# Kernel tuning notes

Hardware: AMD Instinct MI355X
Metric: run time of the kernel (lower is better)

Reference implementation:

```python
import jax, jax.numpy as jnp
import numpy as np

DIM = 2048
H = 16        # num query heads
HK = 2        # num kv heads
D = DIM // H  # head_dim = 128
G = H // HK   # q heads per kv head = 8
SCALE = 1.0 / np.sqrt(D)


def setup_inputs() -> dict:
    key = jax.random.key(0)
    ks = jax.random.split(key, 9)
    xavier = lambda k, fi, fo: jax.random.uniform(k, (fi, fo), jnp.float32,
                                                  -np.sqrt(6.0 / (fi + fo)), np.sqrt(6.0 / (fi + fo)))
    return {
        "x": jax.random.normal(ks[0], (2, 2048, DIM), jnp.float32),
        "Wq": xavier(ks[1], DIM, H * D),  "bq": jnp.zeros((H * D,), jnp.float32),
        "Wk": xavier(ks[2], DIM, HK * D), "bk": jnp.zeros((HK * D,), jnp.float32),
        "Wv": xavier(ks[3], DIM, HK * D), "bv": jnp.zeros((HK * D,), jnp.float32),
        "Wo": xavier(ks[4], H * D, DIM),  "bo": jnp.zeros((DIM,), jnp.float32),
    }


def reference(x, Wq, bq, Wk, bk, Wv, bv, Wo, bo):
    B, T, C = x.shape
    # projections; q grouped as (kv_head, group) so repeat_interleave becomes a broadcast
    q = (x @ Wq + bq).reshape(B, T, HK, G, D)   # [B,T,Hk,G,D]
    k = (x @ Wk + bk).reshape(B, T, HK, D)      # [B,T,Hk,D]
    v = (x @ Wv + bv).reshape(B, T, HK, D)
    # scores: [B,Hk,G,Tq,Tk] — shared K broadcast across the G query heads per kv head
    scores = jnp.einsum('bqhgd,bshd->bhgqs', q, k) * SCALE
    scores = jnp.clip(scores, -100.0, 100.0)
    attn = jax.nn.softmax(scores, axis=-1)
    out = jnp.einsum('bhgqs,bshd->bqhgd', attn, v).reshape(B, T, H * D)
    return out @ Wo + bo
```

## Files before the change

kernel.cpp:

```cpp
#include <hip/hip_runtime.h>
#include <cstdint>

typedef __bf16 bf16x8 __attribute__((ext_vector_type(8)));
typedef float floatx4 __attribute__((ext_vector_type(4)));
typedef unsigned short u16;
typedef unsigned int u32;

#define SCALE2 0.1275434297677098f
#define CLIP2  144.26950408889634f

__device__ __forceinline__ u16 f2bf(float f) {
  union { float f; u32 i; } v; v.f = f;
  u32 r = v.i + 0x7fffu + ((v.i >> 16) & 1u);
  return (u16)(r >> 16);
}

__device__ __forceinline__ void gll16(const void* g, void* l) {
  __builtin_amdgcn_global_load_lds(
      (const __attribute__((address_space(1))) u32*)g,
      (__attribute__((address_space(3))) u32*)l, 16, 0, 0);
}

__global__ __launch_bounds__(256) void convert_bf16(
    const float* __restrict__ src, u16* __restrict__ dst, int n4) {
  int i = blockIdx.x * 256 + threadIdx.x;
  if (i >= n4) return;
  float4 v = ((const float4*)src)[i];
  ushort4 o;
  o.x = f2bf(v.x); o.y = f2bf(v.y); o.z = f2bf(v.z); o.w = f2bf(v.w);
  ((ushort4*)dst)[i] = o;
}

__global__ __launch_bounds__(256) void transpose_cat(
    const float* __restrict__ W0, const float* __restrict__ W1,
    const float* __restrict__ W2,
    int n1, int n2, int ld0, int ld1, int ld2, int K, u16* __restrict__ Bt) {
  __shared__ u16 tile[32][33];
  const int k0 = blockIdx.x * 32, n0 = blockIdx.y * 32;
  const float* src; int ld, nb;
  if (n0 < n1)      { src = W0; ld = ld0; nb = n0; }
  else if (n0 < n2) { src = W1; ld = ld1; nb = n0 - n1; }
  else              { src = W2; ld = ld2; nb = n0 - n2; }
  const int tx = threadIdx.x, ty = threadIdx.y;
#pragma unroll
  for (int i = 0; i < 4; i++) {
    int k = ty + i * 8;
    tile[k][tx] = f2bf(src[(size_t)(k0 + k) * ld + nb + tx]);
  }
  __syncthreads();
#pragma unroll
  for (int i = 0; i < 4; i++) {
    int n = ty + i * 8;
    Bt[(size_t)(n0 + n) * K + k0 + tx] = tile[tx][n];
  }
}

template <int EPI>
__global__ __launch_bounds__(256) void gemm_bt(
    const u16* __restrict__ A, const u16* __restrict__ Bt,
    const float* __restrict__ bias0, const float* __restrict__ bias1,
    const float* __restrict__ bias2,
    u16* __restrict__ out0, u16* __restrict__ out1, u16* __restrict__ out2,
    float* __restrict__ outf,
    int M, int N, int K) {
  __shared__ u16 As[2][128][32];
  __shared__ u16 Bs[2][128][32];
  const int tid  = threadIdx.x;
  const int w    = tid >> 6, L = tid & 63, ln = L & 15, quad = L >> 4;
  const int m0   = blockIdx.y * 128, n0 = blockIdx.x * 128;
  const int mw   = (w & 1) * 64, nw = (w >> 1) * 64;
  const int sr = w * 32 + (L >> 2), sc = (L & 3) * 8;
  const u16* ga = &A [(size_t)(m0 + sr) * K + sc];
  const u16* gb = &Bt[(size_t)(n0 + sr) * K + sc];
  floatx4 acc[4][4] = {};
  const int nk = K >> 5;

  gll16(ga, &As[0][w * 32][0]);
  gll16(ga + (size_t)16 * K, &As[0][w * 32 + 16][0]);
  gll16(gb, &Bs[0][w * 32][0]);
  gll16(gb + (size_t)16 * K, &Bs[0][w * 32 + 16][0]);

  for (int i = 0; i < nk; i++) {
    const int cur = i & 1;
    __syncthreads();
    if (i + 1 < nk) {
      const int kt = (i + 1) << 5;
      gll16(ga + kt, &As[cur ^ 1][w * 32][0]);
      gll16(ga + (size_t)16 * K + kt, &As[cur ^ 1][w * 32 + 16][0]);
      gll16(gb + kt, &Bs[cur ^ 1][w * 32][0]);
      gll16(gb + (size_t)16 * K + kt, &Bs[cur ^ 1][w * 32 + 16][0]);
    }
    bf16x8 af[4], bf[4];
#pragma unroll
    for (int mb = 0; mb < 4; mb++) af[mb] = *(const bf16x8*)&As[cur][mw + mb * 16 + ln][quad * 8];
#pragma unroll
    for (int nb = 0; nb < 4; nb++) bf[nb] = *(const bf16x8*)&Bs[cur][nw + nb * 16 + ln][quad * 8];
#pragma unroll
    for (int mb = 0; mb < 4; mb++)
#pragma unroll
      for (int nb = 0; nb < 4; nb++)
        acc[mb][nb] = __builtin_amdgcn_mfma_f32_16x16x32_bf16(af[mb], bf[nb], acc[mb][nb], 0, 0, 0);
  }

#pragma unroll
  for (int mb = 0; mb < 4; mb++) {
#pragma unroll
    for (int nb = 0; nb < 4; nb++) {
#pragma unroll
      for (int r = 0; r < 4; r++) {
        const int m = m0 + mw + mb * 16 + quad * 4 + r;
        const int n = n0 + nw + nb * 16 + ln;
        float v = acc[mb][nb][r];
        if constexpr (EPI == 0) {
          if (n < 2048) {
            v = (v + bias0[n]) * SCALE2;
            out0[(size_t)m * 2048 + n] = f2bf(v);
          } else if (n < 2304) {
            const int j = n - 2048;
            v += bias1[j];
            out1[(size_t)m * 256 + j] = f2bf(v);
          } else {
            const int j = n - 2304;
            v += bias2[j];
            const int b = m >> 11, t = m & 2047;
            out2[((size_t)(b * 256 + j)) * 2048 + t] = f2bf(v);
          }
        } else {
          v += bias0[n];
          outf[(size_t)m * (size_t)N + n] = v;
        }
      }
    }
  }
}

__global__ __launch_bounds__(512, 4) void attn_kernel(
    const u16* __restrict__ Q, const u16* __restrict__ K,
    const u16* __restrict__ Vt, u16* __restrict__ O) {
  __shared__ u16 Ksh[2][16 * 512];
  __shared__ u16 Vsh[2][16 * 512];
  const int tid = threadIdx.x;
  const int w = tid >> 6, L = tid & 63, ln = L & 15, quad = L >> 4;
  const int qt = blockIdx.x, h = blockIdx.y, b = blockIdx.z;
  const int hk = h >> 3;
  const size_t qrow0 = (size_t)b * 2048 + qt * 128 + w * 16;

  const u16* Kbase = K + (size_t)b * 2048 * 256 + hk * 128;
  const u16* Vbase = Vt + (size_t)(b * 2 + hk) * 128 * 2048;

  const int fk0 = w * 2;
  const int kkc0 = fk0 >> 2, knb0 = fk0 & 3;
  const int kkc1 = (fk0 + 1) >> 2, knb1 = (fk0 + 1) & 3;
  const int vkc0 = fk0 >> 3, vnb0 = fk0 & 7;
  const int vkc1 = (fk0 + 1) >> 3, vnb1 = (fk0 + 1) & 7;
  const u16* gK0 = Kbase + (size_t)(knb0 * 16 + ln) * 256 + kkc0 * 32 + quad * 8;
  const u16* gK1 = Kbase + (size_t)(knb1 * 16 + ln) * 256 + kkc1 * 32 + quad * 8;
  const u16* gV0 = Vbase + (size_t)(vnb0 * 16 + ln) * 2048 + vkc0 * 32 + quad * 8;
  const u16* gV1 = Vbase + (size_t)(vnb1 * 16 + ln) * 2048 + vkc1 * 32 + quad * 8;

  bf16x8 qf[4];
#pragma unroll
  for (int kc = 0; kc < 4; kc++)
    qf[kc] = *(const bf16x8*)&Q[(qrow0 + ln) * 2048 + h * 128 + kc * 32 + quad * 8];

  floatx4 oT[8] = {};
  float mrow = -1e30f, lrow = 0.f;

  gll16(gK0, &Ksh[0][(size_t)fk0 * 512]);
  gll16(gK1, &Ksh[0][(size_t)(fk0 + 1) * 512]);
  gll16(gV0, &Vsh[0][(size_t)fk0 * 512]);
  gll16(gV1, &Vsh[0][(size_t)(fk0 + 1) * 512]);

  const int s0l = ((L & 16) << 1) + ln;
  const int s1l = s0l + 16;
  const bool hi = (L & 32) != 0;

  for (int i = 0; i < 32; i++) {
    const int cur = i & 1;
    __syncthreads();
    if (i < 31) {
      const int s0 = (i + 1) * 64;
      gll16(gK0 + (size_t)s0 * 256, &Ksh[cur ^ 1][(size_t)fk0 * 512]);
      gll16(gK1 + (size_t)s0 * 256, &Ksh[cur ^ 1][(size_t)(fk0 + 1) * 512]);
      gll16(gV0 + s0, &Vsh[cur ^ 1][(size_t)fk0 * 512]);
      gll16(gV1 + s0, &Vsh[cur ^ 1][(size_t)(fk0 + 1) * 512]);
    }

    floatx4 sf[4] = {};
#pragma unroll
    for (int kc = 0; kc < 4; kc++) {
#pragma unroll
      for (int nb = 0; nb < 4; nb++) {
        bf16x8 kf = *(const bf16x8*)&Ksh[cur][(size_t)(kc * 4 + nb) * 512 + L * 8];
        sf[nb] = __builtin_amdgcn_mfma_f32_16x16x32_bf16(kf, qf[kc], sf[nb], 0, 0, 0);
      }
    }
#pragma unroll
    for (int nb = 0; nb < 4; nb++)
#pragma unroll
      for (int r = 0; r < 4; r++)
        sf[nb][r] = __builtin_amdgcn_fmed3f(sf[nb][r], -CLIP2, CLIP2);

    float mx = sf[0][0];
#pragma unroll
    for (int nb = 0; nb < 4; nb++)
#pragma unroll
      for (int r = 0; r < 4; r++) mx = fmaxf(mx, sf[nb][r]);
    mx = fmaxf(mx, __shfl_xor(mx, 16));
    mx = fmaxf(mx, __shfl_xor(mx, 32));
    const float mn = fmaxf(mrow, mx);
    const float alpha = __builtin_amdgcn_exp2f(mrow - mn);
    mrow = mn;

    float s = 0.f;
    uint2 pk[4];
#pragma unroll
    for (int nb = 0; nb < 4; nb++) {
      float p0 = __builtin_amdgcn_exp2f(sf[nb][0] - mn);
      float p1 = __builtin_amdgcn_exp2f(sf[nb][1] - mn);
      float p2 = __builtin_amdgcn_exp2f(sf[nb][2] - mn);
      float p3 = __builtin_amdgcn_exp2f(sf[nb][3] - mn);
      s += (p0 + p1) + (p2 + p3);
      pk[nb].x = (u32)f2bf(p0) | ((u32)f2bf(p1) << 16);
      pk[nb].y = (u32)f2bf(p2) | ((u32)f2bf(p3) << 16);
    }
    s += __shfl_xor(s, 16);
    s += __shfl_xor(s, 32);
    lrow = lrow * alpha + s;

    if (__ballot(alpha < 1.f)) {
#pragma unroll
      for (int nb = 0; nb < 8; nb++)
#pragma unroll
        for (int r = 0; r < 4; r++) oT[nb][r] *= alpha;
    }

#pragma unroll
    for (int kc = 0; kc < 2; kc++) {
      u32 a0 = pk[2 * kc].x, a1 = pk[2 * kc].y;
      u32 b0 = pk[2 * kc + 1].x, b1 = pk[2 * kc + 1].y;
      u32 t00 = __shfl(a0, s0l), t01 = __shfl(a1, s0l);
      u32 t02 = __shfl(a0, s1l), t03 = __shfl(a1, s1l);
      u32 t10 = __shfl(b0, s0l), t11 = __shfl(b1, s0l);
      u32 t12 = __shfl(b0, s1l), t13 = __shfl(b1, s1l);
      union { u32 u[4]; bf16x8 v; } pb;
      pb.u[0] = hi ? t10 : t00;
      pb.u[1] = hi ? t11 : t01;
      pb.u[2] = hi ? t12 : t02;
      pb.u[3] = hi ? t13 : t03;
#pragma unroll
      for (int nb = 0; nb < 8; nb++) {
        bf16x8 vf = *(const bf16x8*)&Vsh[cur][(size_t)(kc * 8 + nb) * 512 + L * 8];
        oT[nb] = __builtin_amdgcn_mfma_f32_16x16x32_bf16(vf, pb.v, oT[nb], 0, 0, 0);
      }
    }
  }

  const float inv = 1.f / lrow;
  u16* orow = O + (qrow0 + ln) * 2048 + h * 128;
#pragma unroll
  for (int nb = 0; nb < 8; nb++)
#pragma unroll
    for (int r = 0; r < 4; r++)
      orow[nb * 16 + quad * 4 + r] = f2bf(oT[nb][r] * inv);
}

extern "C" void kernel_launch(void* const* d_in, const int* in_sizes, int n_in,
                              void* d_out, int out_size, void* d_ws, size_t ws_size,
                              hipStream_t stream) {
  const float* x  = (const float*)d_in[0];
  const float* Wq = (const float*)d_in[1];
  const float* bq = (const float*)d_in[2];
  const float* Wk = (const float*)d_in[3];
  const float* bk = (const float*)d_in[4];
  const float* Wv = (const float*)d_in[5];
  const float* bv = (const float*)d_in[6];
  const float* Wo = (const float*)d_in[7];
  const float* bo = (const float*)d_in[8];
  float* out = (float*)d_out;

  char* ws = (char*)d_ws;
  u16* xb     = (u16*)(ws);
  u16* Ob     = (u16*)(ws);
  u16* Wqkv_t = (u16*)(ws + 16777216);
  u16* Wot    = (u16*)(ws + 27262976);
  u16* Qb     = (u16*)(ws + 35651584);
  u16* Kb     = (u16*)(ws + 52428800);
  u16* Vtb    = (u16*)(ws + 54525952);
  (void)in_sizes; (void)n_in; (void)out_size; (void)ws_size;

  convert_bf16<<<8192, 256, 0, stream>>>(x, xb, 2097152);

  transpose_cat<<<dim3(64, 80), dim3(32, 8), 0, stream>>>(
      Wq, Wk, Wv, 2048, 2304, 2048, 256, 256, 2048, Wqkv_t);
  transpose_cat<<<dim3(64, 64), dim3(32, 8), 0, stream>>>(
      Wo, Wo, Wo, 2048, 2048, 2048, 2048, 2048, 2048, Wot);

  gemm_bt<0><<<dim3(20, 32), 256, 0, stream>>>(
      xb, Wqkv_t, bq, bk, bv, Qb, Kb, Vtb, nullptr, 4096, 2560, 2048);

  attn_kernel<<<dim3(16, 16, 2), 512, 0, stream>>>(Qb, Kb, Vtb, Ob);

  gemm_bt<1><<<dim3(16, 32), 256, 0, stream>>>(
      Ob, Wot, bo, nullptr, nullptr, nullptr, nullptr, nullptr, out, 4096, 2048, 2048);
}
```

Before: 344.6 us.

## Switch attention to 32x32x16 MFMA with 4 waves and lazy softmax rescale

New measurement: 337.3 us. -2.1%, faster.

```diff
diff --git a/kernel.cpp b/kernel.cpp
--- a/kernel.cpp
+++ b/kernel.cpp
@@ -3,16 +3,24 @@
 
 typedef __bf16 bf16x8 __attribute__((ext_vector_type(8)));
 typedef float floatx4 __attribute__((ext_vector_type(4)));
+typedef float floatx16 __attribute__((ext_vector_type(16)));
 typedef unsigned short u16;
 typedef unsigned int u32;
 
 #define SCALE2 0.1275434297677098f
 #define CLIP2  144.26950408889634f
+#define DEFER  8.0f
 
 __device__ __forceinline__ u16 f2bf(float f) {
   union { float f; u32 i; } v; v.f = f;
   u32 r = v.i + 0x7fffu + ((v.i >> 16) & 1u);
   return (u16)(r >> 16);
+}
+
+__device__ __forceinline__ u32 cvtpk(float lo, float hi) {
+  u32 r;
+  asm("v_cvt_pk_bf16_f32 %0, %1, %2" : "=v"(r) : "v"(lo), "v"(hi));
+  return r;
 }
 
 __device__ __forceinline__ void gll16(const void* g, void* l) {
@@ -134,124 +142,120 @@
   }
 }
 
-__global__ __launch_bounds__(512, 4) void attn_kernel(
+__global__ __launch_bounds__(256, 2) void attn_kernel(
     const u16* __restrict__ Q, const u16* __restrict__ K,
     const u16* __restrict__ Vt, u16* __restrict__ O) {
   __shared__ u16 Ksh[2][16 * 512];
   __shared__ u16 Vsh[2][16 * 512];
   const int tid = threadIdx.x;
-  const int w = tid >> 6, L = tid & 63, ln = L & 15, quad = L >> 4;
+  const int w = tid >> 6, L = tid & 63;
+  const int ln = L & 31, hf = L >> 5;
   const int qt = blockIdx.x, h = blockIdx.y, b = blockIdx.z;
   const int hk = h >> 3;
-  const size_t qrow0 = (size_t)b * 2048 + qt * 128 + w * 16;
+  const size_t qrow0 = (size_t)b * 2048 + qt * 128 + w * 32;
 
   const u16* Kbase = K + (size_t)b * 2048 * 256 + hk * 128;
   const u16* Vbase = Vt + (size_t)(b * 2 + hk) * 128 * 2048;
 
-  const int fk0 = w * 2;
-  const int kkc0 = fk0 >> 2, knb0 = fk0 & 3;
-  const int kkc1 = (fk0 + 1) >> 2, knb1 = (fk0 + 1) & 3;
-  const int vkc0 = fk0 >> 3, vnb0 = fk0 & 7;
-  const int vkc1 = (fk0 + 1) >> 3, vnb1 = (fk0 + 1) & 7;
-  const u16* gK0 = Kbase + (size_t)(knb0 * 16 + ln) * 256 + kkc0 * 32 + quad * 8;
-  const u16* gK1 = Kbase + (size_t)(knb1 * 16 + ln) * 256 + kkc1 * 32 + quad * 8;
-  const u16* gV0 = Vbase + (size_t)(vnb0 * 16 + ln) * 2048 + vkc0 * 32 + quad * 8;
-  const u16* gV1 = Vbase + (size_t)(vnb1 * 16 + ln) * 2048 + vkc1 * 32 + quad * 8;
-
-  bf16x8 qf[4];
-#pragma unroll
-  for (int kc = 0; kc < 4; kc++)
-    qf[kc] = *(const bf16x8*)&Q[(qrow0 + ln) * 2048 + h * 128 + kc * 32 + quad * 8];
-
-  floatx4 oT[8] = {};
+  const u16* gK[4];
+  const u16* gV[4];
+#pragma unroll
+  for (int j = 0; j < 4; j++) {
+    const int fK = 4 * w + j, mb = fK >> 3, kc = fK & 7;
+    gK[j] = Kbase + (size_t)(mb * 32 + ln) * 256 + kc * 16 + hf * 8;
+    const int fV = 4 * w + j, db = fV >> 2, ks = fV & 3;
+    gV[j] = Vbase + (size_t)(db * 32 + ln) * 2048 + ks * 16 + hf * 8;
+  }
+
+  bf16x8 qf[8];
+#pragma unroll
+  for (int kc = 0; kc < 8; kc++)
+    qf[kc] = *(const bf16x8*)&Q[(qrow0 + ln) * 2048 + h * 128 + kc * 16 + hf * 8];
+
+  floatx16 oT[4] = {};
   float mrow = -1e30f, lrow = 0.f;
 
-  gll16(gK0, &Ksh[0][(size_t)fk0 * 512]);
-  gll16(gK1, &Ksh[0][(size_t)(fk0 + 1) * 512]);
-  gll16(gV0, &Vsh[0][(size_t)fk0 * 512]);
-  gll16(gV1, &Vsh[0][(size_t)(fk0 + 1) * 512]);
-
-  const int s0l = ((L & 16) << 1) + ln;
-  const int s1l = s0l + 16;
-  const bool hi = (L & 32) != 0;
+#pragma unroll
+  for (int j = 0; j < 4; j++) {
+    gll16(gK[j], &Ksh[0][(4 * w + j) * 512]);
+    gll16(gV[j], &Vsh[0][(4 * w + j) * 512]);
+  }
 
   for (int i = 0; i < 32; i++) {
     const int cur = i & 1;
     __syncthreads();
     if (i < 31) {
-      const int s0 = (i + 1) * 64;
-      gll16(gK0 + (size_t)s0 * 256, &Ksh[cur ^ 1][(size_t)fk0 * 512]);
-      gll16(gK1 + (size_t)s0 * 256, &Ksh[cur ^ 1][(size_t)(fk0 + 1) * 512]);
-      gll16(gV0 + s0, &Vsh[cur ^ 1][(size_t)fk0 * 512]);
-      gll16(gV1 + s0, &Vsh[cur ^ 1][(size_t)(fk0 + 1) * 512]);
-    }
-
-    floatx4 sf[4] = {};
-#pragma unroll
-    for (int kc = 0; kc < 4; kc++) {
-#pragma unroll
-      for (int nb = 0; nb < 4; nb++) {
-        bf16x8 kf = *(const bf16x8*)&Ksh[cur][(size_t)(kc * 4 + nb) * 512 + L * 8];
-        sf[nb] = __builtin_amdgcn_mfma_f32_16x16x32_bf16(kf, qf[kc], sf[nb], 0, 0, 0);
-      }
-    }
-#pragma unroll
-    for (int nb = 0; nb < 4; nb++)
-#pragma unroll
-      for (int r = 0; r < 4; r++)
-        sf[nb][r] = __builtin_amdgcn_fmed3f(sf[nb][r], -CLIP2, CLIP2);
-
-    float mx = sf[0][0];
-#pragma unroll
-    for (int nb = 0; nb < 4; nb++)
-#pragma unroll
-      for (int r = 0; r < 4; r++) mx = fmaxf(mx, sf[nb][r]);
-    mx = fmaxf(mx, __shfl_xor(mx, 16));
+#pragma unroll
+      for (int j = 0; j < 4; j++) {
+        gll16(gK[j] + (size_t)(i + 1) * 64 * 256, &Ksh[cur ^ 1][(4 * w + j) * 512]);
+        gll16(gV[j] + (size_t)(i + 1) * 64, &Vsh[cur ^ 1][(4 * w + j) * 512]);
+      }
+    }
+
+    floatx16 sf[2] = {};
+#pragma unroll
+    for (int kc = 0; kc < 8; kc++) {
+#pragma unroll
+      for (int mb = 0; mb < 2; mb++) {
+        bf16x8 kf = *(const bf16x8*)&Ksh[cur][(mb * 8 + kc) * 512 + L * 8];
+        sf[mb] = __builtin_amdgcn_mfma_f32_32x32x16_bf16(kf, qf[kc], sf[mb], 0, 0, 0);
+      }
+    }
+
+    float mx = -1e30f;
+#pragma unroll
+    for (int mb = 0; mb < 2; mb++)
+#pragma unroll
+      for (int r = 0; r < 16; r++) {
+        sf[mb][r] = __builtin_amdgcn_fmed3f(sf[mb][r], -CLIP2, CLIP2);
+        mx = fmaxf(mx, sf[mb][r]);
+      }
     mx = fmaxf(mx, __shfl_xor(mx, 32));
-    const float mn = fmaxf(mrow, mx);
-    const float alpha = __builtin_amdgcn_exp2f(mrow - mn);
-    mrow = mn;
+
+    const bool need = __ballot(mx > mrow + DEFER) != 0;
+    float mn = mrow;
+    float alpha = 1.f;
+    if (need) {
+      mn = fmaxf(mrow, mx);
+      alpha = __builtin_amdgcn_exp2f(mrow - mn);
+      mrow = mn;
+    }
 
     float s = 0.f;
-    uint2 pk[4];
-#pragma unroll
-    for (int nb = 0; nb < 4; nb++) {
-      float p0 = __builtin_amdgcn_exp2f(sf[nb][0] - mn);
-      float p1 = __builtin_amdgcn_exp2f(sf[nb][1] - mn);
-      float p2 = __builtin_amdgcn_exp2f(sf[nb][2] - mn);
-      float p3 = __builtin_amdgcn_exp2f(sf[nb][3] - mn);
-      s += (p0 + p1) + (p2 + p3);
-      pk[nb].x = (u32)f2bf(p0) | ((u32)f2bf(p1) << 16);
-      pk[nb].y = (u32)f2bf(p2) | ((u32)f2bf(p3) << 16);
-    }
-    s += __shfl_xor(s, 16);
+#pragma unroll
+    for (int mb = 0; mb < 2; mb++)
+#pragma unroll
+      for (int r = 0; r < 16; r++) {
+        const float p = __builtin_amdgcn_exp2f(sf[mb][r] - mn);
+        sf[mb][r] = p;
+        s += p;
+      }
     s += __shfl_xor(s, 32);
-    lrow = lrow * alpha + s;
-
-    if (__ballot(alpha < 1.f)) {
-#pragma unroll
-      for (int nb = 0; nb < 8; nb++)
-#pragma unroll
-        for (int r = 0; r < 4; r++) oT[nb][r] *= alpha;
-    }
-
-#pragma unroll
-    for (int kc = 0; kc < 2; kc++) {
-      u32 a0 = pk[2 * kc].x, a1 = pk[2 * kc].y;
-      u32 b0 = pk[2 * kc + 1].x, b1 = pk[2 * kc + 1].y;
-      u32 t00 = __shfl(a0, s0l), t01 = __shfl(a1, s0l);
-      u32 t02 = __shfl(a0, s1l), t03 = __shfl(a1, s1l);
-      u32 t10 = __shfl(b0, s0l), t11 = __shfl(b1, s0l);
-      u32 t12 = __shfl(b0, s1l), t13 = __shfl(b1, s1l);
+    if (need) {
+      lrow = lrow * alpha + s;
+#pragma unroll
+      for (int db = 0; db < 4; db++)
+#pragma unroll
+        for (int r = 0; r < 16; r++) oT[db][r] *= alpha;
+    } else {
+      lrow += s;
+    }
+
+#pragma unroll
+    for (int ks = 0; ks < 4; ks++) {
+      const int mb = ks >> 1, s8 = (ks & 1) * 8;
+      u32 cA0 = cvtpk(sf[mb][s8 + 0], sf[mb][s8 + 1]);
+      u32 cA1 = cvtpk(sf[mb][s8 + 2], sf[mb][s8 + 3]);
+      u32 cB0 = cvtpk(sf[mb][s8 + 4], sf[mb][s8 + 5]);
+      u32 cB1 = cvtpk(sf[mb][s8 + 6], sf[mb][s8 + 7]);
+      asm("v_permlane32_swap_b32 %0, %1" : "+v"(cA0), "+v"(cB0));
+      asm("v_permlane32_swap_b32 %0, %1" : "+v"(cA1), "+v"(cB1));
       union { u32 u[4]; bf16x8 v; } pb;
-      pb.u[0] = hi ? t10 : t00;
-      pb.u[1] = hi ? t11 : t01;
-      pb.u[2] = hi ? t12 : t02;
-      pb.u[3] = hi ? t13 : t03;
-#pragma unroll
-      for (int nb = 0; nb < 8; nb++) {
-        bf16x8 vf = *(const bf16x8*)&Vsh[cur][(size_t)(kc * 8 + nb) * 512 + L * 8];
-        oT[nb] = __builtin_amdgcn_mfma_f32_16x16x32_bf16(vf, pb.v, oT[nb], 0, 0, 0);
+      pb.u[0] = cA0; pb.u[1] = cA1; pb.u[2] = cB0; pb.u[3] = cB1;
+#pragma unroll
+      for (int db = 0; db < 4; db++) {
+        bf16x8 vf = *(const bf16x8*)&Vsh[cur][(db * 4 + ks) * 512 + L * 8];
+        oT[db] = __builtin_amdgcn_mfma_f32_32x32x16_bf16(vf, pb.v, oT[db], 0, 0, 0);
       }
     }
   }
@@ -259,10 +263,15 @@
   const float inv = 1.f / lrow;
   u16* orow = O + (qrow0 + ln) * 2048 + h * 128;
 #pragma unroll
-  for (int nb = 0; nb < 8; nb++)
-#pragma unroll
-    for (int r = 0; r < 4; r++)
-      orow[nb * 16 + quad * 4 + r] = f2bf(oT[nb][r] * inv);
+  for (int db = 0; db < 4; db++) {
+#pragma unroll
+    for (int g = 0; g < 4; g++) {
+      uint2 st;
+      st.x = cvtpk(oT[db][g * 4 + 0] * inv, oT[db][g * 4 + 1] * inv);
+      st.y = cvtpk(oT[db][g * 4 + 2] * inv, oT[db][g * 4 + 3] * inv);
+      *(uint2*)&orow[db * 32 + g * 8 + hf * 4] = st;
+    }
+  }
 }
 
 extern "C" void kernel_launch(void* const* d_in, const int* in_sizes, int n_in,
@@ -299,7 +308,7 @@
   gemm_bt<0><<<dim3(20, 32), 256, 0, stream>>>(
       xb, Wqkv_t, bq, bk, bv, Qb, Kb, Vtb, nullptr, 4096, 2560, 2048);
 
-  attn_kernel<<<dim3(16, 16, 2), 512, 0, stream>>>(Qb, Kb, Vtb, Ob);
+  attn_kernel<<<dim3(16, 16, 2), 256, 0, stream>>>(Qb, Kb, Vtb, Ob);
 
   gemm_bt<1><<<dim3(16, 32), 256, 0, stream>>>(
       Ob, Wot, bo, nullptr, nullptr, nullptr, nullptr, nullptr, out, 4096, 2048, 2048);
```
